# Kernel optimization log

Measured on AMD Instinct MI355X. Metric: run time of the kernel, lower is better.

## Reference

```python
import jax, jax.numpy as jnp
import numpy as np
from math import sqrt


def _attention(q, k, v, scale):
    # q: [B, L, H, E], k: [B, S, H, E], v: [B, S, H, D]
    scores = jnp.einsum('blhe,bshe->bhls', q, k)
    A = jax.nn.softmax(scale * scores, axis=-1)           # [B, H, L, S]
    V = jnp.einsum('bhls,bshd->blhd', A, v)               # [B, L, H, D]
    B, L, H, D = V.shape
    return V.reshape(B, L, H * D)


def setup_inputs() -> dict:
    key = jax.random.key(0)
    ks = jax.random.split(key, 6)
    shape = (4, 2048, 8, 64)  # [B, L, H, E]
    names = ['queries_w', 'keys_w', 'values_w', 'queries_m', 'keys_m', 'values_m']
    inp = {n: jax.random.normal(k, shape, dtype=jnp.float32) for n, k in zip(names, ks)}
    inp['attn_mask'] = jnp.zeros((1,), dtype=bool)  # unused by the module
    return inp


def reference(queries_w, keys_w, values_w, queries_m, keys_m, values_m, attn_mask):
    E = queries_w.shape[-1]
    scale = 1.0 / sqrt(E)
    c0 = _attention(queries_w, keys_w, values_w, scale)   # w -> w
    c1 = _attention(queries_m, keys_m, values_m, scale)   # m -> m
    c2 = _attention(queries_w, keys_m, values_m, scale)   # w -> m
    c3 = _attention(queries_m, keys_w, values_w, scale)   # m -> w
    return (c0, c1, c2, c3)
```

## Files before the change

kernel.cpp:

```cpp
#include <hip/hip_runtime.h>


typedef _Float16 half8 __attribute__((ext_vector_type(8)));
typedef _Float16 half4 __attribute__((ext_vector_type(4)));
typedef _Float16 half2t __attribute__((ext_vector_type(2)));
typedef float f32x4 __attribute__((ext_vector_type(4)));

#define MFMA_QK(a, b, c) __builtin_amdgcn_mfma_f32_16x16x32_f16(a, b, c, 0, 0, 0)
#define MFMA_PV(a, b, c) __builtin_amdgcn_mfma_f32_16x16x16f16(a, b, c, 0, 0, 0)

static __device__ inline half2t pk(float a, float b) {
    return __builtin_bit_cast(half2t, __builtin_amdgcn_cvt_pkrtz(a, b));
}

#define QSCALE 0.1803368867f

#define TENS_ELEMS 4194304

__global__ __launch_bounds__(256) void prep_kernel(
    const float* __restrict__ kw, const float* __restrict__ km,
    const float* __restrict__ vw, const float* __restrict__ vm,
    _Float16* __restrict__ wsK, _Float16* __restrict__ wsV)
{
    const int t = blockIdx.x, bh = blockIdx.y, z = blockIdx.z;
    const int set = z & 1;
    const int b = bh >> 3, h = bh & 7;
    const int tid = threadIdx.x;
    const size_t headOff = ((size_t)b * 2048) * 512 + (size_t)h * 64;
    const size_t tileOff = ((((size_t)set * 32 + bh) * 32) + t) * 4096;

    __shared__ _Float16 T[64 * 68];

    if (z < 2) {
        const float* kb = (set ? km : kw) + headOff;
        _Float16* dst = wsK + tileOff;
#pragma unroll
        for (int w = 0; w < 2; ++w) {
            const int c = tid + w * 256;
            const int l16 = c & 15, q = (c >> 4) & 3, kc = (c >> 6) & 1, nb = (c >> 7) & 3;
            const float* p = kb + (size_t)(t * 64 + nb * 16 + l16) * 512 + kc * 32 + q * 8;
            float4 x = *(const float4*)p;
            float4 y = *(const float4*)(p + 4);
            half2t h0 = pk(x.x * QSCALE, x.y * QSCALE), h1 = pk(x.z * QSCALE, x.w * QSCALE);
            half2t h2 = pk(y.x * QSCALE, y.y * QSCALE), h3 = pk(y.z * QSCALE, y.w * QSCALE);
            half8 o = {h0.x, h0.y, h1.x, h1.y, h2.x, h2.y, h3.x, h3.y};
            *(half8*)(dst + (size_t)c * 8) = o;
        }
    } else {
        const float* vb = (set ? vm : vw) + headOff;
        const int s_row = tid >> 2, cg = (tid & 3) * 16;
        const float* row = vb + (size_t)(t * 64 + s_row) * 512 + cg;
#pragma unroll
        for (int k4 = 0; k4 < 4; ++k4) {
            float4 v = *(const float4*)(row + k4 * 4);
            const int d0 = cg + k4 * 4;
            T[(d0 + 0) * 68 + s_row] = (_Float16)v.x;
            T[(d0 + 1) * 68 + s_row] = (_Float16)v.y;
            T[(d0 + 2) * 68 + s_row] = (_Float16)v.z;
            T[(d0 + 3) * 68 + s_row] = (_Float16)v.w;
        }
        __syncthreads();
        _Float16* dst = wsV + tileOff;
#pragma unroll
        for (int w = 0; w < 2; ++w) {
            const int c = tid + w * 256;
            const int lane = c & 63, db = (c >> 6) & 3, m = (c >> 8) & 1;
            const int l16 = lane & 15, q = lane >> 4;
            const _Float16* tp = &T[(db * 16 + l16) * 68 + m * 32 + q * 4];
            half4 a = *(const half4*)tp;
            half4 b2 = *(const half4*)(tp + 16);
            half8 o = {a[0], a[1], a[2], a[3], b2[0], b2[1], b2[2], b2[3]};
            *(half8*)(dst + (size_t)c * 8) = o;
        }
    }
}

__global__ __launch_bounds__(256, 4) void bm_attn_main(
    const float* __restrict__ qw, const float* __restrict__ qm,
    const _Float16* __restrict__ wsK, const _Float16* __restrict__ wsV,
    float* __restrict__ out)
{
    const int ltile = blockIdx.x, bh = blockIdx.y, set = blockIdx.z;
    const int b = bh >> 3, h = bh & 7;
    const float* Q0 = set ? qm : qw;
    const float* Q1 = set ? qw : qm;
    const int c0 = set ? 1 : 0, c1 = set ? 2 : 3;

    const int tid = threadIdx.x;
    const int wave = tid >> 6, lane = tid & 63;
    const int quad = lane >> 4, l16 = lane & 15;

    const size_t headOff = ((size_t)b * 2048) * 512 + (size_t)h * 64;
    const size_t tileBase = (((size_t)set * 32 + bh) * 32) * 4096;
    const _Float16* kp = wsK + tileBase + lane * 8;
    const _Float16* vp = wsV + tileBase + lane * 8;

    const int rowBase = ltile * 64 + wave * 16;
    half8 qB[2][2];
    {
        const float* qs[2] = { Q0 + headOff, Q1 + headOff };
#pragma unroll
        for (int s = 0; s < 2; ++s)
#pragma unroll
            for (int kc = 0; kc < 2; ++kc) {
                const float* p = qs[s] + (size_t)(rowBase + l16) * 512 + kc * 32 + quad * 8;
                float4 x = *(const float4*)p;
                float4 y = *(const float4*)(p + 4);
                half2t h0 = pk(x.x, x.y), h1 = pk(x.z, x.w);
                half2t h2 = pk(y.x, y.y), h3 = pk(y.z, y.w);
                qB[s][kc] = (half8){h0.x, h0.y, h1.x, h1.y, h2.x, h2.y, h3.x, h3.y};
            }
    }

    f32x4 accO[2][4];
    f32x4 rsD[2];
#pragma unroll
    for (int s = 0; s < 2; ++s) {
        rsD[s] = (f32x4){0.f, 0.f, 0.f, 0.f};
#pragma unroll
        for (int d = 0; d < 4; ++d) accO[s][d] = (f32x4){0.f, 0.f, 0.f, 0.f};
    }
    const half8 ones8 = {(_Float16)1.f, (_Float16)1.f, (_Float16)1.f, (_Float16)1.f,
                         (_Float16)1.f, (_Float16)1.f, (_Float16)1.f, (_Float16)1.f};

#pragma unroll 1
    for (int tile = 0; tile < 32; ++tile) {
        const _Float16* kt = kp + (size_t)tile * 4096;
        const _Float16* vt = vp + (size_t)tile * 4096;
#pragma unroll
        for (int m = 0; m < 2; ++m) {
            const _Float16* kb0 = kt + (size_t)(m * 4) * 512;
            half8 k00 = *(const half8*)(kb0 + 0 * 512);
            half8 k01 = *(const half8*)(kb0 + 1 * 512);
            half8 k10 = *(const half8*)(kb0 + 2 * 512);
            half8 k11 = *(const half8*)(kb0 + 3 * 512);
            f32x4 z = {0.f, 0.f, 0.f, 0.f};
            f32x4 s00 = MFMA_QK(k00, qB[0][0], z);
            s00 = MFMA_QK(k01, qB[0][1], s00);
            f32x4 s01 = MFMA_QK(k10, qB[0][0], z);
            s01 = MFMA_QK(k11, qB[0][1], s01);
            f32x4 s10 = MFMA_QK(k00, qB[1][0], z);
            s10 = MFMA_QK(k01, qB[1][1], s10);
            f32x4 s11 = MFMA_QK(k10, qB[1][0], z);
            s11 = MFMA_QK(k11, qB[1][1], s11);

            half2t a0 = pk(__builtin_amdgcn_exp2f(s00[0]), __builtin_amdgcn_exp2f(s00[1]));
            half2t a1 = pk(__builtin_amdgcn_exp2f(s00[2]), __builtin_amdgcn_exp2f(s00[3]));
            half2t a2 = pk(__builtin_amdgcn_exp2f(s01[0]), __builtin_amdgcn_exp2f(s01[1]));
            half2t a3 = pk(__builtin_amdgcn_exp2f(s01[2]), __builtin_amdgcn_exp2f(s01[3]));
            half8 pa0 = {a0.x, a0.y, a1.x, a1.y, a2.x, a2.y, a3.x, a3.y};
            half2t b0 = pk(__builtin_amdgcn_exp2f(s10[0]), __builtin_amdgcn_exp2f(s10[1]));
            half2t b1 = pk(__builtin_amdgcn_exp2f(s10[2]), __builtin_amdgcn_exp2f(s10[3]));
            half2t b2 = pk(__builtin_amdgcn_exp2f(s11[0]), __builtin_amdgcn_exp2f(s11[1]));
            half2t b3 = pk(__builtin_amdgcn_exp2f(s11[2]), __builtin_amdgcn_exp2f(s11[3]));
            half8 pa1 = {b0.x, b0.y, b1.x, b1.y, b2.x, b2.y, b3.x, b3.y};

            rsD[0] = MFMA_QK(pa0, ones8, rsD[0]);
            rsD[1] = MFMA_QK(pa1, ones8, rsD[1]);

            const _Float16* vb0 = vt + (size_t)(m * 4) * 512;
#pragma unroll
            for (int db = 0; db < 4; ++db) {
                half8 bv = *(const half8*)(vb0 + db * 512);
                accO[0][db] = MFMA_QK(pa0, bv, accO[0][db]);
                accO[1][db] = MFMA_QK(pa1, bv, accO[1][db]);
            }
        }
    }

#pragma unroll
    for (int s = 0; s < 2; ++s) {
        const int c = (s == 0) ? c0 : c1;
        float* ob = out + (size_t)c * TENS_ELEMS + headOff;
#pragma unroll
        for (int r = 0; r < 4; ++r) {
            const float inv = 1.0f / rsD[s][r];
            const int row = rowBase + quad * 4 + r;
#pragma unroll
            for (int db = 0; db < 4; ++db) {
                ob[(size_t)row * 512 + db * 16 + l16] = accO[s][db][r] * inv;
            }
        }
    }
}

__global__ __launch_bounds__(256) void bm_attn_fallback(
    const float* __restrict__ qw, const float* __restrict__ kw, const float* __restrict__ vw,
    const float* __restrict__ qm, const float* __restrict__ km, const float* __restrict__ vm,
    float* __restrict__ out)
{
    const int ltile = blockIdx.x, bh = blockIdx.y, set = blockIdx.z;
    const int b = bh >> 3, h = bh & 7;
    const float* Q0 = set ? qm : qw;
    const float* Q1 = set ? qw : qm;
    const int c0 = set ? 1 : 0, c1 = set ? 2 : 3;
    const int tid = threadIdx.x;
    const int wave = tid >> 6, lane = tid & 63;
    const int quad = lane >> 4, l16 = lane & 15;
    __shared__ __align__(16) _Float16 Kt[64 * 72];
    __shared__ __align__(16) _Float16 Vt[64 * 72];
    const size_t headOff = ((size_t)b * 2048) * 512 + (size_t)h * 64;
    const float* kb = (set ? km : kw) + headOff;
    const float* vb = (set ? vm : vw) + headOff;
    const int rowBase = ltile * 64 + wave * 16;
    half8 qB[2][2];
    {
        const float* qs[2] = { Q0 + headOff, Q1 + headOff };
#pragma unroll
        for (int s = 0; s < 2; ++s)
#pragma unroll
            for (int kc = 0; kc < 2; ++kc) {
                const float* p = qs[s] + (size_t)(rowBase + l16) * 512 + kc * 32 + quad * 8;
                half8 q;
#pragma unroll
                for (int j = 0; j < 8; ++j) q[j] = (_Float16)(p[j] * QSCALE);
                qB[s][kc] = q;
            }
    }
    f32x4 accO[2][4];
#pragma unroll
    for (int s = 0; s < 2; ++s)
#pragma unroll
        for (int d = 0; d < 4; ++d) accO[s][d] = (f32x4){0.f, 0.f, 0.f, 0.f};
    float rs0 = 0.f, rs1 = 0.f;
#pragma unroll 1
    for (int tile = 0; tile < 32; ++tile) {
        const int s0 = tile * 64;
        __syncthreads();
        {
            const int r0 = tid >> 4, f4 = (tid & 15) * 4;
#pragma unroll
            for (int p4 = 0; p4 < 4; ++p4) {
                const int row = p4 * 16 + r0;
                float4 v = *(const float4*)(kb + (size_t)(s0 + row) * 512 + f4);
                half2t a = pk(v.x, v.y), b2 = pk(v.z, v.w);
                half4 o = {a.x, a.y, b2.x, b2.y};
                *(half4*)&Kt[row * 72 + f4] = o;
            }
            const int sl = tid & 63, dq = tid >> 6;
            const float* vrow = vb + (size_t)(s0 + sl) * 512;
#pragma unroll
            for (int i = 0; i < 4; ++i) {
                const int d0 = dq * 16 + i * 4;
                float4 v = *(const float4*)(vrow + d0);
                Vt[(d0 + 0) * 72 + sl] = (_Float16)v.x;
                Vt[(d0 + 1) * 72 + sl] = (_Float16)v.y;
                Vt[(d0 + 2) * 72 + sl] = (_Float16)v.z;
                Vt[(d0 + 3) * 72 + sl] = (_Float16)v.w;
            }
        }
        __syncthreads();
#pragma unroll
        for (int nb = 0; nb < 4; ++nb) {
            half8 k0 = *(const half8*)&Kt[(nb * 16 + l16) * 72 + quad * 8];
            half8 k1 = *(const half8*)&Kt[(nb * 16 + l16) * 72 + 32 + quad * 8];
            f32x4 z = {0.f, 0.f, 0.f, 0.f};
            f32x4 st0 = MFMA_QK(k0, qB[0][0], z);
            st0 = MFMA_QK(k1, qB[0][1], st0);
            f32x4 st1 = MFMA_QK(k0, qB[1][0], z);
            st1 = MFMA_QK(k1, qB[1][1], st1);
            half2t p00 = pk(__builtin_amdgcn_exp2f(st0[0]), __builtin_amdgcn_exp2f(st0[1]));
            half2t p01 = pk(__builtin_amdgcn_exp2f(st0[2]), __builtin_amdgcn_exp2f(st0[3]));
            half2t p10 = pk(__builtin_amdgcn_exp2f(st1[0]), __builtin_amdgcn_exp2f(st1[1]));
            half2t p11 = pk(__builtin_amdgcn_exp2f(st1[2]), __builtin_amdgcn_exp2f(st1[3]));
            rs0 += (float)p00.x + (float)p00.y + (float)p01.x + (float)p01.y;
            rs1 += (float)p10.x + (float)p10.y + (float)p11.x + (float)p11.y;
            half4 ph0 = {p00.x, p00.y, p01.x, p01.y};
            half4 ph1 = {p10.x, p10.y, p11.x, p11.y};
#pragma unroll
            for (int db = 0; db < 4; ++db) {
                half4 bv = *(const half4*)&Vt[(db * 16 + l16) * 72 + nb * 16 + quad * 4];
                accO[0][db] = MFMA_PV(ph0, bv, accO[0][db]);
                accO[1][db] = MFMA_PV(ph1, bv, accO[1][db]);
            }
        }
    }
#pragma unroll
    for (int s = 0; s < 2; ++s) {
        float rs = (s == 0) ? rs0 : rs1;
        rs += __shfl_xor(rs, 16);
        rs += __shfl_xor(rs, 32);
        const float inv = 1.0f / rs;
        const int c = (s == 0) ? c0 : c1;
        float* ob = out + (size_t)c * TENS_ELEMS + headOff;
#pragma unroll
        for (int r = 0; r < 4; ++r) {
            const float invr = __shfl(inv, quad * 4 + r);
            const int row = rowBase + quad * 4 + r;
#pragma unroll
            for (int db = 0; db < 4; ++db) {
                ob[(size_t)row * 512 + db * 16 + l16] = accO[s][db][r] * invr;
            }
        }
    }
}

extern "C" void kernel_launch(void* const* d_in, const int* in_sizes, int n_in,
                              void* d_out, int out_size, void* d_ws, size_t ws_size,
                              hipStream_t stream) {
    const float* qw = (const float*)d_in[0];
    const float* kw = (const float*)d_in[1];
    const float* vw = (const float*)d_in[2];
    const float* qm = (const float*)d_in[3];
    const float* km = (const float*)d_in[4];
    const float* vm = (const float*)d_in[5];
    float* out = (float*)d_out;

    dim3 block(256);
    const size_t NEED = (size_t)4 * TENS_ELEMS * sizeof(_Float16);

    if (ws_size >= NEED) {
        _Float16* wsK = (_Float16*)d_ws;
        _Float16* wsV = wsK + (size_t)2 * TENS_ELEMS;
        prep_kernel<<<dim3(32, 32, 4), block, 0, stream>>>(kw, km, vw, vm, wsK, wsV);
        bm_attn_main<<<dim3(32, 32, 2), block, 0, stream>>>(qw, qm, wsK, wsV, out);
    } else {
        bm_attn_fallback<<<dim3(32, 32, 2), block, 0, stream>>>(qw, kw, vw, qm, km, vm, out);
    }
}
```

Baseline: 307.7 us.

## Double-buffer K/V tiles in LDS via async global_load_lds

Instead of each wave reading K/V fragments straight from global memory, the block stages each 4096-element K and V tile into shared memory with direct global-to-LDS loads. Two buffers are used so the next tile is prefetched while the current one is consumed. This lets the four waves share one copy of each tile and overlaps the loads with MFMA work, at the cost of 32KB LDS per block and a block barrier every tile, which can limit occupancy. Correctness relies on the barrier covering the async LDS writes (vmcnt waiting).

Result: faster. 277.2 us (-9.9%).

```diff
diff --git a/kernel.cpp b/kernel.cpp
--- a/kernel.cpp
+++ b/kernel.cpp
@@ -11,6 +11,12 @@
 
 static __device__ inline half2t pk(float a, float b) {
     return __builtin_bit_cast(half2t, __builtin_amdgcn_cvt_pkrtz(a, b));
+}
+
+static __device__ __forceinline__ void gload_lds16(const _Float16* g, _Float16* l) {
+    __builtin_amdgcn_global_load_lds(
+        (const __attribute__((address_space(1))) unsigned int*)g,
+        (__attribute__((address_space(3))) unsigned int*)l, 16, 0, 0);
 }
 
 #define QSCALE 0.1803368867f
@@ -90,10 +96,13 @@
     const int wave = tid >> 6, lane = tid & 63;
     const int quad = lane >> 4, l16 = lane & 15;
 
+    __shared__ __align__(16) _Float16 ldsK[2][4096];
+    __shared__ __align__(16) _Float16 ldsV[2][4096];
+
     const size_t headOff = ((size_t)b * 2048) * 512 + (size_t)h * 64;
     const size_t tileBase = (((size_t)set * 32 + bh) * 32) * 4096;
-    const _Float16* kp = wsK + tileBase + lane * 8;
-    const _Float16* vp = wsV + tileBase + lane * 8;
+    const _Float16* tK = wsK + tileBase;
+    const _Float16* tV = wsV + tileBase;
 
     const int rowBase = ltile * 64 + wave * 16;
     half8 qB[2][2];
@@ -123,13 +132,30 @@
     const half8 ones8 = {(_Float16)1.f, (_Float16)1.f, (_Float16)1.f, (_Float16)1.f,
                          (_Float16)1.f, (_Float16)1.f, (_Float16)1.f, (_Float16)1.f};
 
+    auto stage = [&](int t, int buf) {
+        const _Float16* gK = tK + (size_t)t * 4096 + tid * 8;
+        const _Float16* gV = tV + (size_t)t * 4096 + tid * 8;
+        _Float16* lK = &ldsK[buf][wave * 512];
+        _Float16* lV = &ldsV[buf][wave * 512];
+        gload_lds16(gK, lK);
+        gload_lds16(gK + 2048, lK + 2048);
+        gload_lds16(gV, lV);
+        gload_lds16(gV + 2048, lV + 2048);
+    };
+
+    stage(0, 0);
+    __syncthreads();
+    int cur = 0;
+
 #pragma unroll 1
     for (int tile = 0; tile < 32; ++tile) {
-        const _Float16* kt = kp + (size_t)tile * 4096;
-        const _Float16* vt = vp + (size_t)tile * 4096;
+        if (tile + 1 < 32) stage(tile + 1, cur ^ 1);
+
+        const _Float16* kt = &ldsK[cur][lane * 8];
+        const _Float16* vt = &ldsV[cur][lane * 8];
 #pragma unroll
         for (int m = 0; m < 2; ++m) {
-            const _Float16* kb0 = kt + (size_t)(m * 4) * 512;
+            const _Float16* kb0 = kt + (m * 4) * 512;
             half8 k00 = *(const half8*)(kb0 + 0 * 512);
             half8 k01 = *(const half8*)(kb0 + 1 * 512);
             half8 k10 = *(const half8*)(kb0 + 2 * 512);
@@ -158,7 +184,7 @@
             rsD[0] = MFMA_QK(pa0, ones8, rsD[0]);
             rsD[1] = MFMA_QK(pa1, ones8, rsD[1]);
 
-            const _Float16* vb0 = vt + (size_t)(m * 4) * 512;
+            const _Float16* vb0 = vt + (m * 4) * 512;
 #pragma unroll
             for (int db = 0; db < 4; ++db) {
                 half8 bv = *(const half8*)(vb0 + db * 512);
@@ -166,6 +192,8 @@
                 accO[1][db] = MFMA_QK(pa1, bv, accO[1][db]);
             }
         }
+        __syncthreads();
+        cur ^= 1;
     }
 
 #pragma unroll
```
